# Performance work log

Hardware: AMD Instinct MI355X
Metric: run time of the kernel (lower is better)

The kernel has to match this reference:

```python
import jax, jax.numpy as jnp
import numpy as np

N_NODES = 512
EMB = 64
TIME_LAG = 8
TIME_LOG = 5.0
EPS = 1e-6
LN_EPS = 1e-5


def _linear(x, w, b):
    return x @ w.T + b


def _lrelu(x):
    return jax.nn.leaky_relu(x, 0.01)


def _layer_norm(x, g, b):
    m = x.mean(-1, keepdims=True)
    v = jnp.var(x, axis=-1, keepdims=True)
    return (x - m) * jax.lax.rsqrt(v + LN_EPS) * g + b


def _forward(skill_seq, time_seq, label_seq, adj, node_embeddings,
             msg_fc1_w, msg_fc1_b, msg_fc2_w, msg_fc2_b,
             f_w1, f_b1, f_ln1_g, f_ln1_b, f_w2, f_b2, f_ln2_g, f_ln2_b, f_w3, f_b3):
    bs, T = skill_seq.shape
    L = TIME_LAG
    steps = T - L
    N, E = N_NODES, EMB

    # emb_history == 0 label remap: 0 -> -1, -1 -> 0, 1 -> 1
    lp = jnp.where(label_seq == 0, -2, label_seq)
    lp = jnp.where(lp == -1, 0, lp)
    lp = jnp.where(lp == -2, -1, lp)

    tf = time_seq.astype(jnp.float32)
    delta_t = jnp.log(jnp.abs(tf[:, :, None] - tf[:, None, :]) + EPS) / jnp.log(TIME_LOG)  # [bs,T,T]

    # initial hidden: scatter last-occurrence embedding of each skill in warmup window
    s0 = skill_seq[:, :L]
    emb_init = node_embeddings[s0] * lp[:, :L, None].astype(jnp.float32)  # [bs,L,E]
    eq = s0[:, :, None] == s0[:, None, :]
    later = jnp.triu(jnp.ones((L, L), bool), 1)
    is_last = ~jnp.any(eq & later, axis=2)  # [bs,L] True at last occurrence
    hidden0 = jnp.zeros((bs, N, E), jnp.float32).at[jnp.arange(bs)[:, None], s0].add(
        emb_init * is_last[..., None])

    # spatial adjacency stack [adj, adj^2/N], batch-major [bs,K,2,N,N]
    adj2 = jnp.matmul(adj, adj) / N
    asp = jnp.transpose(jnp.stack([adj, adj2], axis=2), (1, 0, 2, 3, 4))

    win = jnp.arange(steps)[:, None] + jnp.arange(L)[None, :]  # [steps,L], entry = t-L+i
    sh_all = skill_seq[:, win]                                  # [bs,steps,L]
    tgt_all = skill_seq[:, L:]                                  # [bs,steps]
    b3 = jnp.arange(bs)[:, None, None]
    # delta_t.transpose(-1,-2)[:, t, t-L:t] == delta_t[:, t-L:t, t]
    dtw_all = delta_t[b3, win[None], (jnp.arange(steps) + L)[None, :, None]]  # [bs,steps,L]

    b_col = jnp.arange(bs)[:, None]
    b_row = jnp.arange(bs)

    def step(hidden, x):
        sh, dtw, tgt = x  # [bs,L], [bs,L], [bs]
        hh = hidden[b_col, sh]  # [bs,L,E]
        # cross_weight = adj_spatial[:, arange(bs), :, skill_history] -> [bs,K,2,L,N]
        cw = jnp.take_along_axis(asp, sh[:, None, None, :, None], axis=3)
        pre = jnp.concatenate([
            jnp.broadcast_to(hh[:, :, None, :], (bs, L, N, E)),
            jnp.broadcast_to(hidden[:, None, :, :], (bs, L, N, E)),
        ], axis=-1)  # [bs,L,N,2E]
        msg = jnp.tanh(_linear(pre, msg_fc1_w, msg_fc1_b))
        msg = jnp.tanh(_linear(msg, msg_fc2_w, msg_fc2_b))  # [bs,L,N,E]
        msg = msg * jnp.exp(-dtw)[:, :, None, None]          # fold time decay into msg
        # sum over spatial hop s and lag l without materializing [bs,K,2,L,N,E]
        agg = jnp.einsum('bksln,blne->bkne', cw, msg)        # [bs,K,N,E]
        new_hidden = agg.mean(axis=1)
        # final MLP (causica-style generate_fully_connected):
        # res(Linear+LReLU), res(LN+Linear+LReLU), LN, Linear -> 2
        h = agg + _lrelu(_linear(agg, f_w1, f_b1))
        h = h + _lrelu(_linear(_layer_norm(h, f_ln1_g, f_ln1_b), f_w2, f_b2))
        logits = _linear(_layer_norm(h, f_ln2_g, f_ln2_b), f_w3, f_b3)  # [bs,K,N,2]
        p = jax.nn.softmax(logits, axis=-1)
        pred = p[b_row, :, tgt, 1:]  # [bs,K,1]
        return new_hidden, pred

    xs = (jnp.transpose(sh_all, (1, 0, 2)), jnp.transpose(dtw_all, (1, 0, 2)), tgt_all.T)
    _, preds = jax.lax.scan(step, hidden0, xs)
    return preds  # [steps, bs, K, 1]


def setup_inputs() -> dict:
    key = jax.random.key(0)
    ks = jax.random.split(key, 12)
    bs, T, N, E, K = 16, 20, N_NODES, EMB, 2
    return {
        'skill_seq': jax.random.randint(ks[0], (bs, T), 0, N),
        'time_seq': jnp.sort(jax.random.randint(ks[1], (bs, T), 0, 100000), axis=-1),
        'label_seq': jax.random.randint(ks[2], (bs, T), 0, 2),
        'adj': jax.random.uniform(ks[3], (K, bs, N, N), jnp.float32),
        'node_embeddings': jax.random.normal(ks[4], (N, E), jnp.float32),
        'msg_fc1_w': jax.random.normal(ks[5], (E, 2 * E), jnp.float32) / np.sqrt(2 * E).astype(np.float32),
        'msg_fc1_b': jnp.zeros((E,), jnp.float32),
        'msg_fc2_w': jax.random.normal(ks[6], (E, E), jnp.float32) / np.sqrt(E).astype(np.float32),
        'msg_fc2_b': jnp.zeros((E,), jnp.float32),
        'f_w1': jax.random.normal(ks[7], (E, E), jnp.float32) / np.sqrt(E).astype(np.float32),
        'f_b1': jnp.zeros((E,), jnp.float32),
        'f_ln1_g': jnp.ones((E,), jnp.float32),
        'f_ln1_b': jnp.zeros((E,), jnp.float32),
        'f_w2': jax.random.normal(ks[8], (E, E), jnp.float32) / np.sqrt(E).astype(np.float32),
        'f_b2': jnp.zeros((E,), jnp.float32),
        'f_ln2_g': jnp.ones((E,), jnp.float32),
        'f_ln2_b': jnp.zeros((E,), jnp.float32),
        'f_w3': jax.random.normal(ks[9], (2, E), jnp.float32) / np.sqrt(E).astype(np.float32),
        'f_b3': jnp.zeros((2,), jnp.float32),
    }


def reference(skill_seq, time_seq, label_seq, adj, node_embeddings,
              msg_fc1_w, msg_fc1_b, msg_fc2_w, msg_fc2_b,
              f_w1, f_b1, f_ln1_g, f_ln1_b, f_w2, f_b2, f_ln2_g, f_ln2_b, f_w3, f_b3):
    return _forward(skill_seq, time_seq, label_seq, adj, node_embeddings,
                    msg_fc1_w, msg_fc1_b, msg_fc2_w, msg_fc2_b,
                    f_w1, f_b1, f_ln1_g, f_ln1_b, f_w2, f_b2, f_ln2_g, f_ln2_b, f_w3, f_b3)
```

## Files before the change

### kernel.cpp

```cpp
#include <hip/hip_runtime.h>
#include <hip/hip_bf16.h>

#define BS 16
#define TT 20
#define STEPS 12
#define NN 512
#define EE 64

typedef __attribute__((ext_vector_type(8))) short bfrag8;
typedef __attribute__((ext_vector_type(4))) float f32x4;
typedef unsigned short ushort_t;
typedef unsigned int uint_t;

#define MFMA16(a,b,c) __builtin_amdgcn_mfma_f32_16x16x32_bf16(a,b,c,0,0,0)

#if __has_builtin(__builtin_amdgcn_rcpf)
#define RCP(x) __builtin_amdgcn_rcpf(x)
#else
#define RCP(x) (1.0f/(x))
#endif

__device__ __forceinline__ float tanh_fast(float x) {
  float t = __expf(-2.f * fabsf(x));
  float r = (1.f - t) * RCP(1.f + t);
  return copysignf(r, x);
}

__device__ __forceinline__ float lrelu(float x) { return x > 0.f ? x : 0.01f * x; }

__device__ __forceinline__ float wsum64(float x) {
  #pragma unroll
  for (int off = 32; off > 0; off >>= 1) x += __shfl_xor(x, off);
  return x;
}

__device__ __forceinline__ ushort_t f2bf(float f) {
  uint_t u = __float_as_uint(f);
  u += 0x7fffu + ((u >> 16) & 1u);
  return (ushort_t)(u >> 16);
}

__global__ __launch_bounds__(256) void setup_kernel(
    const int* __restrict__ skill, const float* __restrict__ adj,
    float* __restrict__ crow)
{
  __shared__ __align__(16) float a_rows[19*516];
  __shared__ __align__(16) float a_cols[5*516];
  __shared__ float red[95*2];
  __shared__ int s_node[5];

  int tid = threadIdx.x, bid = blockIdx.x;
  int kb = bid >> 2, pq = bid & 3;
  int b = kb & 15;
  const float* A = adj + (size_t)kb*NN*NN;

  for (int idx = tid; idx < 19*512; idx += 256) {
    int tpos = idx >> 9, m = idx & 511;
    a_rows[tpos*516 + m] = A[(size_t)skill[b*TT + tpos]*NN + m];
  }
  if (tid < 5) s_node[tid] = skill[b*TT + pq*5 + tid];
  __syncthreads();
  for (int idx = tid; idx < 5*512; idx += 256) {
    int p = idx >> 9, m = idx & 511;
    a_cols[p*516 + m] = A[(size_t)m*NN + s_node[p]];
  }
  __syncthreads();

  int pr = tid & 127, mh = tid >> 7;
  if (pr < 95) {
    int tpos = pr / 5, p = pr % 5;
    const float4* ra = (const float4*)&a_rows[tpos*516 + mh*256];
    const float4* rc = (const float4*)&a_cols[p*516 + mh*256];
    float s = 0.f;
    #pragma unroll 8
    for (int i = 0; i < 64; ++i) {
      float4 x = ra[i], y = rc[i];
      s += x.x*y.x + x.y*y.y + x.z*y.z + x.w*y.w;
    }
    red[pr*2 + mh] = s;
  }
  __syncthreads();
  if (tid < 95) {
    int tpos = tid / 5, p = tid % 5;
    float dot = red[tid*2] + red[tid*2 + 1];
    crow[(size_t)kb*380 + tpos*20 + pq*5 + p] =
        a_rows[tpos*516 + s_node[p]] + dot * (1.f/512.f);
  }
}

__global__ __launch_bounds__(512) void step_kernel(
    const int* __restrict__ skill, const int* __restrict__ timeq,
    const int* __restrict__ label, const float* __restrict__ nemb,
    const float* __restrict__ W1, const float* __restrict__ W2,
    const float* __restrict__ b1, const float* __restrict__ b2,
    const float* __restrict__ crow,
    const float* __restrict__ fw1, const float* __restrict__ fb1,
    const float* __restrict__ g1, const float* __restrict__ be1,
    const float* __restrict__ fw2, const float* __restrict__ fb2,
    const float* __restrict__ g2, const float* __restrict__ be2,
    const float* __restrict__ fw3, const float* __restrict__ fb3,
    float* __restrict__ out)
{
  __shared__ __align__(16) ushort_t sWa[64*72];
  __shared__ __align__(16) ushort_t sWb[64*72];
  __shared__ __align__(16) ushort_t sW2[64*72];
  __shared__ __align__(16) ushort_t sH[32*72];
  __shared__ __align__(16) float sFP[28*72];
  __shared__ __align__(16) ushort_t sM1[160*72];
  __shared__ float sCROW[2*19*20];
  __shared__ float sED[STEPS*8];
  __shared__ float sAGG[24*68];
  __shared__ int sSK[TT];

  int tid = threadIdx.x, b = blockIdx.x;
  int w = tid >> 6, lane = tid & 63, q = lane >> 4, nn = lane & 15;
  int ct = w & 3, half = w >> 2, epos = ct*16 + nn;

  if (tid < TT) sSK[tid] = skill[b*TT + tid];
  for (int idx = tid; idx < 4096; idx += 512) {
    int e = idx >> 6, j = idx & 63;
    sWa[e*72 + j] = f2bf(W1[e*128 + j]);
    sWb[e*72 + j] = f2bf(W1[e*128 + 64 + j]);
    sW2[e*72 + j] = f2bf(W2[e*64 + j]);
  }
  for (int idx = tid; idx < 760; idx += 512) {
    int k = idx / 380, r2 = idx % 380;
    sCROW[idx] = crow[(size_t)(k*BS + b)*380 + r2];
  }
  if (tid < STEPS*8) {
    int s = tid >> 3, l = tid & 7;
    float d = fabsf((float)(timeq[b*TT + s + l] - timeq[b*TT + s + 8]));
    sED[tid] = expf(-logf(d + 1e-6f) * 0.6213349345596119f);
  }
  __syncthreads();

  for (int idx = tid; idx < 32*64; idx += 512) {
    int p = idx >> 6, e = idx & 63;
    ushort_t hv = 0;
    if (p < 20) {
      int node = sSK[p];
      int lstar = -1;
      #pragma unroll
      for (int l = 0; l < 8; ++l) if (sSK[l] == node) lstar = l;
      if (lstar >= 0) {
        float lp = (label[b*TT + lstar] == 1) ? 1.f : -1.f;
        hv = f2bf(nemb[node*EE + e] * lp);
      }
    }
    sH[p*72 + e] = hv;
  }
  __syncthreads();

  bfrag8 wb0 = *(const bfrag8*)&sWb[epos*72 + q*8];
  bfrag8 wb1 = *(const bfrag8*)&sWb[epos*72 + 32 + q*8];
  bfrag8 wa0 = *(const bfrag8*)&sWa[epos*72 + q*8];
  bfrag8 wa1 = *(const bfrag8*)&sWa[epos*72 + 32 + q*8];
  bfrag8 w20 = *(const bfrag8*)&sW2[epos*72 + q*8];
  bfrag8 w21 = *(const bfrag8*)&sW2[epos*72 + 32 + q*8];
  float b1v = b1[epos], b2v = b2[epos];

  for (int t = 0; t < STEPS; ++t) {
    if (half == 0) {
      bfrag8 a0 = *(const bfrag8*)&sH[nn*72 + q*8];
      bfrag8 a1 = *(const bfrag8*)&sH[nn*72 + 32 + q*8];
      f32x4 accV = {0,0,0,0};
      accV = MFMA16(a0, wb0, accV);
      accV = MFMA16(a1, wb1, accV);
      int ur = (nn < 8) ? (t + nn) : 24;
      bfrag8 u0 = *(const bfrag8*)&sH[ur*72 + q*8];
      bfrag8 u1 = *(const bfrag8*)&sH[ur*72 + 32 + q*8];
      f32x4 accU = {0,0,0,0};
      accU = MFMA16(u0, wa0, accU);
      accU = MFMA16(u1, wa1, accU);
      #pragma unroll
      for (int r = 0; r < 4; ++r)
        sFP[(q*4 + r)*72 + epos] = tanh_fast(accV[r]);
      if (q < 2) {
        #pragma unroll
        for (int r = 0; r < 4; ++r)
          sFP[(20 + q*4 + r)*72 + epos] = tanh_fast(accU[r] + b1v);
      }
    } else {
      bfrag8 a0 = *(const bfrag8*)&sH[(16 + nn)*72 + q*8];
      bfrag8 a1 = *(const bfrag8*)&sH[(16 + nn)*72 + 32 + q*8];
      f32x4 accV = {0,0,0,0};
      accV = MFMA16(a0, wb0, accV);
      accV = MFMA16(a1, wb1, accV);
      if (q == 0) {
        #pragma unroll
        for (int r = 0; r < 4; ++r)
          sFP[(16 + r)*72 + epos] = tanh_fast(accV[r]);
      }
    }
    __syncthreads();

    {
      int pp = tid >> 5, ep = tid & 31;
      for (int p = pp; p < 20; p += 16) {
        float2 tv2 = *(const float2*)&sFP[p*72 + 2*ep];
        #pragma unroll
        for (int l = 0; l < 8; ++l) {
          float2 tu2 = *(const float2*)&sFP[(20 + l)*72 + 2*ep];
          float2 num, den, m;
          num.x = tu2.x + tv2.x;            num.y = tu2.y + tv2.y;
          den.x = fmaf(tu2.x, tv2.x, 1.f);  den.y = fmaf(tu2.y, tv2.y, 1.f);
          den.x = fmaxf(den.x, 1e-30f);     den.y = fmaxf(den.y, 1e-30f);
          m.x = num.x * RCP(den.x);         m.y = num.y * RCP(den.y);
          __hip_bfloat162 h2 = __float22bfloat162_rn(m);
          *(__hip_bfloat162*)&sM1[(p*8 + l)*72 + 2*ep] = h2;
        }
      }
    }
    __syncthreads();

    const float* edt = &sED[t*8];
    #pragma unroll
    for (int rr = 0; rr < 5; ++rr) {
      int rt = half*5 + rr;
      bfrag8 a0 = *(const bfrag8*)&sM1[(rt*16 + nn)*72 + q*8];
      bfrag8 a1 = *(const bfrag8*)&sM1[(rt*16 + nn)*72 + 32 + q*8];
      f32x4 z = {0,0,0,0};
      z = MFMA16(a0, w20, z);
      z = MFMA16(a1, w21, z);
      int p = rt*2 + (q >> 1);
      float ag0 = 0.f, ag1 = 0.f;
      #pragma unroll
      for (int r = 0; r < 4; ++r) {
        int l = (q & 1)*4 + r;
        float m2 = tanh_fast(z[r] + b2v) * edt[l];
        ag0 = fmaf(sCROW[(t + l)*20 + p], m2, ag0);
        ag1 = fmaf(sCROW[380 + (t + l)*20 + p], m2, ag1);
      }
      ag0 += __shfl_xor(ag0, 16);
      ag1 += __shfl_xor(ag1, 16);
      if ((q & 1) == 0) {
        sH[p*72 + epos] = f2bf(0.5f*(ag0 + ag1));
        if (p == t + 8) {
          sAGG[(t*2 + 0)*68 + epos] = ag0;
          sAGG[(t*2 + 1)*68 + epos] = ag1;
        }
      }
    }
    __syncthreads();
  }

  float* fwLDS = (float*)sM1;
  float* sXN   = sFP;

  for (int idx = tid; idx < 4096; idx += 512)
    fwLDS[(idx >> 6)*65 + (idx & 63)] = fw1[idx];
  __syncthreads();

  int e = lane;
  float h1s[3];
  float fb1v = fb1[e], g1v = g1[e], be1v = be1[e];
  #pragma unroll
  for (int r3 = 0; r3 < 3; ++r3) {
    int task = r3*8 + w;
    const float* xv = &sAGG[task*68];
    float x = xv[e];
    float y = fb1v;
    for (int j = 0; j < 64; ++j) y = fmaf(xv[j], fwLDS[e*65 + j], y);
    float h1 = x + lrelu(y);
    float mean1 = wsum64(h1) * (1.f/64.f);
    float d1 = h1 - mean1;
    float var1 = wsum64(d1*d1) * (1.f/64.f);
    float xn = d1 * rsqrtf(var1 + 1e-5f) * g1v + be1v;
    sXN[task*68 + e] = xn;
    h1s[r3] = h1;
  }
  __syncthreads();

  for (int idx = tid; idx < 4096; idx += 512)
    fwLDS[(idx >> 6)*65 + (idx & 63)] = fw2[idx];
  __syncthreads();

  float fb2v = fb2[e], g2v = g2[e], be2v = be2[e];
  float w3a = fw3[e], w3b = fw3[64 + e];
  float fb30 = fb3[0], fb31 = fb3[1];
  #pragma unroll
  for (int r3 = 0; r3 < 3; ++r3) {
    int task = r3*8 + w;
    const float* xnv = &sXN[task*68];
    float z = fb2v;
    for (int j = 0; j < 64; ++j) z = fmaf(xnv[j], fwLDS[e*65 + j], z);
    float h2 = h1s[r3] + lrelu(z);
    float mean2 = wsum64(h2) * (1.f/64.f);
    float d2 = h2 - mean2;
    float var2 = wsum64(d2*d2) * (1.f/64.f);
    float xn2 = d2 * rsqrtf(var2 + 1e-5f) * g2v + be2v;
    float p0 = wsum64(xn2 * w3a);
    float p1 = wsum64(xn2 * w3b);
    if (e == 0) {
      int ts = task >> 1, kk = task & 1;
      float l0 = p0 + fb30, l1 = p1 + fb31;
      out[(ts*BS + b)*2 + kk] = 1.f / (1.f + expf(l0 - l1));
    }
  }
}

extern "C" void kernel_launch(void* const* d_in, const int* in_sizes, int n_in,
                              void* d_out, int out_size, void* d_ws, size_t ws_size,
                              hipStream_t stream) {
  const int*   skill = (const int*)d_in[0];
  const int*   timeq = (const int*)d_in[1];
  const int*   label = (const int*)d_in[2];
  const float* adj   = (const float*)d_in[3];
  const float* nemb  = (const float*)d_in[4];
  const float* W1    = (const float*)d_in[5];
  const float* b1    = (const float*)d_in[6];
  const float* W2    = (const float*)d_in[7];
  const float* b2    = (const float*)d_in[8];
  float* out = (float*)d_out;

  float* crow = (float*)d_ws;

  setup_kernel<<<128, 256, 0, stream>>>(skill, adj, crow);
  step_kernel<<<16, 512, 0, stream>>>(skill, timeq, label, nemb, W1, W2,
      b1, b2, crow,
      (const float*)d_in[9],  (const float*)d_in[10],
      (const float*)d_in[11], (const float*)d_in[12],
      (const float*)d_in[13], (const float*)d_in[14],
      (const float*)d_in[15], (const float*)d_in[16],
      (const float*)d_in[17], (const float*)d_in[18], out);
}
```

Baseline: 164.4 us.

## Fuse Pade message build into MFMA operands and skip unused node rows per step

```diff
diff --git a/kernel.cpp b/kernel.cpp
--- a/kernel.cpp
+++ b/kernel.cpp
@@ -20,10 +20,15 @@
 #define RCP(x) (1.0f/(x))
 #endif
 
+#if __has_builtin(__builtin_amdgcn_exp2f)
+#define EXP2F(x) __builtin_amdgcn_exp2f(x)
+#else
+#define EXP2F(x) exp2f(x)
+#endif
+
 __device__ __forceinline__ float tanh_fast(float x) {
-  float t = __expf(-2.f * fabsf(x));
-  float r = (1.f - t) * RCP(1.f + t);
-  return copysignf(r, x);
+  float t = EXP2F(x * 2.8853900817779268f);
+  return 1.f - 2.f * RCP(1.f + t);
 }
 
 __device__ __forceinline__ float lrelu(float x) { return x > 0.f ? x : 0.01f * x; }
@@ -38,6 +43,14 @@
   uint_t u = __float_as_uint(f);
   u += 0x7fffu + ((u >> 16) & 1u);
   return (ushort_t)(u >> 16);
+}
+
+__device__ __forceinline__ __hip_bfloat162 pade2(float2 tv, float2 tu) {
+  float nx = tu.x + tv.x, ny = tu.y + tv.y;
+  float dx = fmaf(tu.x, tv.x, 1.f), dy = fmaf(tu.y, tv.y, 1.f);
+  dx = fmaxf(dx, 1e-30f); dy = fmaxf(dy, 1e-30f);
+  float2 m; m.x = nx * RCP(dx); m.y = ny * RCP(dy);
+  return __float22bfloat162_rn(m);
 }
 
 __global__ __launch_bounds__(256) void setup_kernel(
@@ -105,11 +118,14 @@
   __shared__ __align__(16) ushort_t sWb[64*72];
   __shared__ __align__(16) ushort_t sW2[64*72];
   __shared__ __align__(16) ushort_t sH[32*72];
-  __shared__ __align__(16) float sFP[28*72];
-  __shared__ __align__(16) ushort_t sM1[160*72];
+  __shared__ __align__(16) float sTV[20*72];
+  __shared__ __align__(16) float sTU[8*72];
   __shared__ float sCROW[2*19*20];
   __shared__ float sED[STEPS*8];
   __shared__ float sAGG[24*68];
+  __shared__ float sXN[24*68];
+  __shared__ __align__(16) float fwL1[64*66];
+  __shared__ __align__(16) float fwL2[64*66];
   __shared__ int sSK[TT];
 
   int tid = threadIdx.x, b = blockIdx.x;
@@ -122,11 +138,11 @@
     sWa[e*72 + j] = f2bf(W1[e*128 + j]);
     sWb[e*72 + j] = f2bf(W1[e*128 + 64 + j]);
     sW2[e*72 + j] = f2bf(W2[e*64 + j]);
-  }
-  for (int idx = tid; idx < 760; idx += 512) {
-    int k = idx / 380, r2 = idx % 380;
-    sCROW[idx] = crow[(size_t)(k*BS + b)*380 + r2];
-  }
+    fwL1[e*66 + j] = fw1[idx];
+    fwL2[e*66 + j] = fw2[idx];
+  }
+  for (int idx = tid; idx < 760; idx += 512)
+    sCROW[idx] = crow[(size_t)((idx/380)*BS + b)*380 + (idx%380)];
   if (tid < STEPS*8) {
     int s = tid >> 3, l = tid & 7;
     float d = fabsf((float)(timeq[b*TT + s + l] - timeq[b*TT + s + 8]));
@@ -155,11 +171,23 @@
   bfrag8 wb1 = *(const bfrag8*)&sWb[epos*72 + 32 + q*8];
   bfrag8 wa0 = *(const bfrag8*)&sWa[epos*72 + q*8];
   bfrag8 wa1 = *(const bfrag8*)&sWa[epos*72 + 32 + q*8];
-  bfrag8 w20 = *(const bfrag8*)&sW2[epos*72 + q*8];
-  bfrag8 w21 = *(const bfrag8*)&sW2[epos*72 + 32 + q*8];
-  float b1v = b1[epos], b2v = b2[epos];
+  bfrag8 w200 = *(const bfrag8*)&sW2[(0*16+nn)*72 + q*8];
+  bfrag8 w201 = *(const bfrag8*)&sW2[(0*16+nn)*72 + 32 + q*8];
+  bfrag8 w210 = *(const bfrag8*)&sW2[(1*16+nn)*72 + q*8];
+  bfrag8 w211 = *(const bfrag8*)&sW2[(1*16+nn)*72 + 32 + q*8];
+  bfrag8 w220 = *(const bfrag8*)&sW2[(2*16+nn)*72 + q*8];
+  bfrag8 w221 = *(const bfrag8*)&sW2[(2*16+nn)*72 + 32 + q*8];
+  bfrag8 w230 = *(const bfrag8*)&sW2[(3*16+nn)*72 + q*8];
+  bfrag8 w231 = *(const bfrag8*)&sW2[(3*16+nn)*72 + 32 + q*8];
+  float b1v = b1[epos];
+  float b2v0 = b2[nn], b2v1 = b2[16+nn], b2v2 = b2[32+nn], b2v3 = b2[48+nn];
+  const bfrag8 ZB = {0,0,0,0,0,0,0,0};
 
   for (int t = 0; t < STEPS; ++t) {
+    int p0 = (t == 11) ? 19 : t + 1;
+    int R  = (t == 11) ? 1  : 19 - t;
+    int ntiles = (R + 1) >> 1;
+
     if (half == 0) {
       bfrag8 a0 = *(const bfrag8*)&sH[nn*72 + q*8];
       bfrag8 a1 = *(const bfrag8*)&sH[nn*72 + 32 + q*8];
@@ -174,11 +202,11 @@
       accU = MFMA16(u1, wa1, accU);
       #pragma unroll
       for (int r = 0; r < 4; ++r)
-        sFP[(q*4 + r)*72 + epos] = tanh_fast(accV[r]);
+        sTV[(q*4 + r)*72 + epos] = tanh_fast(accV[r]);
       if (q < 2) {
         #pragma unroll
         for (int r = 0; r < 4; ++r)
-          sFP[(20 + q*4 + r)*72 + epos] = tanh_fast(accU[r] + b1v);
+          sTU[(q*4 + r)*72 + epos] = tanh_fast(accU[r] + b1v);
       }
     } else {
       bfrag8 a0 = *(const bfrag8*)&sH[(16 + nn)*72 + q*8];
@@ -189,67 +217,74 @@
       if (q == 0) {
         #pragma unroll
         for (int r = 0; r < 4; ++r)
-          sFP[(16 + r)*72 + epos] = tanh_fast(accV[r]);
+          sTV[(16 + r)*72 + epos] = tanh_fast(accV[r]);
       }
     }
     __syncthreads();
 
-    {
-      int pp = tid >> 5, ep = tid & 31;
-      for (int p = pp; p < 20; p += 16) {
-        float2 tv2 = *(const float2*)&sFP[p*72 + 2*ep];
+    for (int rt = w; rt < ntiles; rt += 8) {
+      int i = rt*2 + (nn >> 3);
+      int lA = nn & 7;
+      bfrag8 a0 = ZB, a1 = ZB;
+      if (i < R) {
+        int p = p0 + i;
+        const float2* tvlo = (const float2*)&sTV[p*72 + q*8];
+        const float2* tvhi = (const float2*)&sTV[p*72 + 32 + q*8];
+        const float2* tulo = (const float2*)&sTU[lA*72 + q*8];
+        const float2* tuhi = (const float2*)&sTU[lA*72 + 32 + q*8];
+        union { bfrag8 v; __hip_bfloat162 h[4]; } A0, A1;
         #pragma unroll
-        for (int l = 0; l < 8; ++l) {
-          float2 tu2 = *(const float2*)&sFP[(20 + l)*72 + 2*ep];
-          float2 num, den, m;
-          num.x = tu2.x + tv2.x;            num.y = tu2.y + tv2.y;
-          den.x = fmaf(tu2.x, tv2.x, 1.f);  den.y = fmaf(tu2.y, tv2.y, 1.f);
-          den.x = fmaxf(den.x, 1e-30f);     den.y = fmaxf(den.y, 1e-30f);
-          m.x = num.x * RCP(den.x);         m.y = num.y * RCP(den.y);
-          __hip_bfloat162 h2 = __float22bfloat162_rn(m);
-          *(__hip_bfloat162*)&sM1[(p*8 + l)*72 + 2*ep] = h2;
+        for (int j = 0; j < 4; ++j) {
+          A0.h[j] = pade2(tvlo[j], tulo[j]);
+          A1.h[j] = pade2(tvhi[j], tuhi[j]);
         }
-      }
-    }
-    __syncthreads();
-
-    const float* edt = &sED[t*8];
-    #pragma unroll
-    for (int rr = 0; rr < 5; ++rr) {
-      int rt = half*5 + rr;
-      bfrag8 a0 = *(const bfrag8*)&sM1[(rt*16 + nn)*72 + q*8];
-      bfrag8 a1 = *(const bfrag8*)&sM1[(rt*16 + nn)*72 + 32 + q*8];
-      f32x4 z = {0,0,0,0};
-      z = MFMA16(a0, w20, z);
-      z = MFMA16(a1, w21, z);
-      int p = rt*2 + (q >> 1);
-      float ag0 = 0.f, ag1 = 0.f;
+        a0 = A0.v; a1 = A1.v;
+      }
+      f32x4 z0 = {0,0,0,0}, z1 = {0,0,0,0}, z2 = {0,0,0,0}, z3 = {0,0,0,0};
+      z0 = MFMA16(a0, w200, z0);  z0 = MFMA16(a1, w201, z0);
+      z1 = MFMA16(a0, w210, z1);  z1 = MFMA16(a1, w211, z1);
+      z2 = MFMA16(a0, w220, z2);  z2 = MFMA16(a1, w221, z2);
+      z3 = MFMA16(a0, w230, z3);  z3 = MFMA16(a1, w231, z3);
+
+      int pi = rt*2 + (q >> 1);
+      int p = p0 + pi;
+      int psafe = (pi < R) ? p : p0;
+      float ag00=0,ag01=0,ag02=0,ag03=0, ag10=0,ag11=0,ag12=0,ag13=0;
       #pragma unroll
       for (int r = 0; r < 4; ++r) {
         int l = (q & 1)*4 + r;
-        float m2 = tanh_fast(z[r] + b2v) * edt[l];
-        ag0 = fmaf(sCROW[(t + l)*20 + p], m2, ag0);
-        ag1 = fmaf(sCROW[380 + (t + l)*20 + p], m2, ag1);
-      }
-      ag0 += __shfl_xor(ag0, 16);
-      ag1 += __shfl_xor(ag1, 16);
-      if ((q & 1) == 0) {
-        sH[p*72 + epos] = f2bf(0.5f*(ag0 + ag1));
+        float c0 = sCROW[(t + l)*20 + psafe];
+        float c1 = sCROW[380 + (t + l)*20 + psafe];
+        float ed = sED[t*8 + l];
+        float m;
+        m = tanh_fast(z0[r] + b2v0) * ed; ag00 = fmaf(c0,m,ag00); ag10 = fmaf(c1,m,ag10);
+        m = tanh_fast(z1[r] + b2v1) * ed; ag01 = fmaf(c0,m,ag01); ag11 = fmaf(c1,m,ag11);
+        m = tanh_fast(z2[r] + b2v2) * ed; ag02 = fmaf(c0,m,ag02); ag12 = fmaf(c1,m,ag12);
+        m = tanh_fast(z3[r] + b2v3) * ed; ag03 = fmaf(c0,m,ag03); ag13 = fmaf(c1,m,ag13);
+      }
+      ag00 += __shfl_xor(ag00,16); ag01 += __shfl_xor(ag01,16);
+      ag02 += __shfl_xor(ag02,16); ag03 += __shfl_xor(ag03,16);
+      ag10 += __shfl_xor(ag10,16); ag11 += __shfl_xor(ag11,16);
+      ag12 += __shfl_xor(ag12,16); ag13 += __shfl_xor(ag13,16);
+      if ((q & 1) == 0 && pi < R) {
+        sH[p*72 +      nn] = f2bf(0.5f*(ag00 + ag10));
+        sH[p*72 + 16 + nn] = f2bf(0.5f*(ag01 + ag11));
+        sH[p*72 + 32 + nn] = f2bf(0.5f*(ag02 + ag12));
+        sH[p*72 + 48 + nn] = f2bf(0.5f*(ag03 + ag13));
         if (p == t + 8) {
-          sAGG[(t*2 + 0)*68 + epos] = ag0;
-          sAGG[(t*2 + 1)*68 + epos] = ag1;
+          sAGG[(t*2 + 0)*68 +      nn] = ag00;
+          sAGG[(t*2 + 0)*68 + 16 + nn] = ag01;
+          sAGG[(t*2 + 0)*68 + 32 + nn] = ag02;
+          sAGG[(t*2 + 0)*68 + 48 + nn] = ag03;
+          sAGG[(t*2 + 1)*68 +      nn] = ag10;
+          sAGG[(t*2 + 1)*68 + 16 + nn] = ag11;
+          sAGG[(t*2 + 1)*68 + 32 + nn] = ag12;
+          sAGG[(t*2 + 1)*68 + 48 + nn] = ag13;
         }
       }
     }
     __syncthreads();
   }
-
-  float* fwLDS = (float*)sM1;
-  float* sXN   = sFP;
-
-  for (int idx = tid; idx < 4096; idx += 512)
-    fwLDS[(idx >> 6)*65 + (idx & 63)] = fw1[idx];
-  __syncthreads();
 
   int e = lane;
   float h1s[3];
@@ -258,10 +293,18 @@
   for (int r3 = 0; r3 < 3; ++r3) {
     int task = r3*8 + w;
     const float* xv = &sAGG[task*68];
+    const float2* xv2 = (const float2*)xv;
+    const float2* wp  = (const float2*)&fwL1[e*66];
     float x = xv[e];
-    float y = fb1v;
-    for (int j = 0; j < 64; ++j) y = fmaf(xv[j], fwLDS[e*65 + j], y);
-    float h1 = x + lrelu(y);
+    float y0 = fb1v, y1 = 0.f;
+    #pragma unroll
+    for (int j = 0; j < 32; j += 2) {
+      float2 a  = xv2[j];     float2 bb = wp[j];
+      y0 = fmaf(a.x, bb.x, y0);  y0 = fmaf(a.y, bb.y, y0);
+      float2 a2 = xv2[j+1];   float2 b2f = wp[j+1];
+      y1 = fmaf(a2.x, b2f.x, y1);  y1 = fmaf(a2.y, b2f.y, y1);
+    }
+    float h1 = x + lrelu(y0 + y1);
     float mean1 = wsum64(h1) * (1.f/64.f);
     float d1 = h1 - mean1;
     float var1 = wsum64(d1*d1) * (1.f/64.f);
@@ -271,29 +314,32 @@
   }
   __syncthreads();
 
-  for (int idx = tid; idx < 4096; idx += 512)
-    fwLDS[(idx >> 6)*65 + (idx & 63)] = fw2[idx];
-  __syncthreads();
-
   float fb2v = fb2[e], g2v = g2[e], be2v = be2[e];
   float w3a = fw3[e], w3b = fw3[64 + e];
   float fb30 = fb3[0], fb31 = fb3[1];
   #pragma unroll
   for (int r3 = 0; r3 < 3; ++r3) {
     int task = r3*8 + w;
-    const float* xnv = &sXN[task*68];
-    float z = fb2v;
-    for (int j = 0; j < 64; ++j) z = fmaf(xnv[j], fwLDS[e*65 + j], z);
-    float h2 = h1s[r3] + lrelu(z);
+    const float2* xn2v = (const float2*)&sXN[task*68];
+    const float2* wp   = (const float2*)&fwL2[e*66];
+    float z0 = fb2v, z1 = 0.f;
+    #pragma unroll
+    for (int j = 0; j < 32; j += 2) {
+      float2 a  = xn2v[j];    float2 bb = wp[j];
+      z0 = fmaf(a.x, bb.x, z0);  z0 = fmaf(a.y, bb.y, z0);
+      float2 a2 = xn2v[j+1];  float2 b2f = wp[j+1];
+      z1 = fmaf(a2.x, b2f.x, z1);  z1 = fmaf(a2.y, b2f.y, z1);
+    }
+    float h2 = h1s[r3] + lrelu(z0 + z1);
     float mean2 = wsum64(h2) * (1.f/64.f);
     float d2 = h2 - mean2;
     float var2 = wsum64(d2*d2) * (1.f/64.f);
     float xn2 = d2 * rsqrtf(var2 + 1e-5f) * g2v + be2v;
-    float p0 = wsum64(xn2 * w3a);
-    float p1 = wsum64(xn2 * w3b);
+    float p0s = wsum64(xn2 * w3a);
+    float p1s = wsum64(xn2 * w3b);
     if (e == 0) {
       int ts = task >> 1, kk = task & 1;
-      float l0 = p0 + fb30, l1 = p1 + fb31;
+      float l0 = p0s + fb30, l1 = p1s + fb31;
       out[(ts*BS + b)*2 + kk] = 1.f / (1.f + expf(l0 - l1));
     }
   }
```

Measured after the change: 157.4 us. -4.3%, faster.
